# Performance work log

Measured on AMD Instinct MI355X. Metric: run time of the kernel, lower is better.

## Reference

```python
import jax, jax.numpy as jnp
import numpy as np

B, A, C_CLS = 64, 9, 20
H_FEAT, W_FEAT = 28, 28
IN_DIM, HID = 1280, 128
N_GT, M_POS = 40, 2048
AC5 = 5 * A + C_CLS


def setup_inputs() -> dict:
    key = jax.random.key(0)
    ks = jax.random.split(key, 10)
    features = jax.random.normal(ks[0], (B, IN_DIM, H_FEAT, W_FEAT), jnp.float32)
    # valid GT boxes in feature-map coordinates: (x1, y1, x2, y2, class)
    x1 = jax.random.uniform(ks[1], (B, N_GT), minval=0.0, maxval=W_FEAT - 6.0)
    y1 = jax.random.uniform(ks[2], (B, N_GT), minval=0.0, maxval=H_FEAT - 6.0)
    bw = jax.random.uniform(ks[3], (B, N_GT), minval=1.0, maxval=5.0)
    bh = jax.random.uniform(ks[4], (B, N_GT), minval=1.0, maxval=5.0)
    cls = jax.random.randint(ks[5], (B, N_GT), 0, C_CLS).astype(jnp.float32)
    bboxes = jnp.stack([x1, y1, x1 + bw, y1 + bh, cls], axis=-1)
    n_anchors_total = B * A * H_FEAT * W_FEAT
    pos_anchor_idx = jax.random.randint(ks[6], (M_POS,), 0, n_anchors_total, dtype=jnp.int32)
    neg_anchor_idx = jax.random.randint(ks[7], (M_POS,), 0, n_anchors_total, dtype=jnp.int32)
    W1 = jax.random.normal(ks[8], (HID, IN_DIM), jnp.float32) * 0.02
    b1 = jnp.zeros((HID,), jnp.float32)
    W2 = jax.random.normal(ks[9], (AC5, HID), jnp.float32) * 0.02
    b2 = jnp.zeros((AC5,), jnp.float32)
    anc = jnp.array([[1.0, 1], [2, 2], [3, 3], [4, 4], [5, 5], [2, 3], [3, 2], [3, 5], [5, 3]], jnp.float32)
    return dict(features=features, bboxes=bboxes, pos_anchor_idx=pos_anchor_idx,
                neg_anchor_idx=neg_anchor_idx, W1=W1, b1=b1, W2=W2, b2=b2, anc=anc)


def _detector_loss(features, bboxes, pos_idx, neg_idx, W1, b1, W2, b2, anc):
    Bx, _, Hf, Wf = features.shape
    N = bboxes.shape[1]
    Mp = pos_idx.shape[0]
    # ---- prediction network: two 1x1 convs (dropout skipped: eval mode) ----
    h = jnp.einsum('bchw,oc->bohw', features, W1) + b1[None, :, None, None]
    h = jax.nn.leaky_relu(h, 0.01)
    x = jnp.einsum('bchw,oc->bohw', h, W2) + b2[None, :, None, None]
    x_anchor = x[:, :5 * A].reshape(Bx, A, 5, Hf, Wf)  # (B,A,5,H,W)
    x_class = x[:, 5 * A:]                              # (B,C,H,W)
    # ---- GenerateGrid + GenerateAnchor ----
    xs = jnp.arange(Wf, dtype=jnp.float32) + 0.5
    ys = jnp.arange(Hf, dtype=jnp.float32) + 0.5
    gx, gy = jnp.meshgrid(xs, ys, indexing='xy')        # both (H,W)
    grid = jnp.stack([gx, gy], axis=-1)                 # (H,W,2)
    half = anc / 2.0                                    # (A,2)
    tl = grid[None] - half[:, None, None]               # (A,H,W,2)
    br = grid[None] + half[:, None, None]
    anchors = jnp.concatenate([tl, br], axis=-1)        # (A,H,W,4)
    p = jnp.broadcast_to(anchors[None], (Bx, A, Hf, Wf, 4)).reshape(Bx, -1, 4)  # (B,M,4)
    # ---- IoU matrix (B, M, N), exactly as source (signed w*h -> positive area) ----
    area_p = ((p[..., 0] - p[..., 2]) * (p[..., 1] - p[..., 3]))[:, :, None]
    area_b = ((bboxes[..., 2] - bboxes[..., 0]) * (bboxes[..., 3] - bboxes[..., 1]))[:, None, :]
    ix1 = jnp.maximum(p[:, :, None, 0], bboxes[:, None, :, 0])
    iy1 = jnp.maximum(p[:, :, None, 1], bboxes[:, None, :, 1])
    ix2 = jnp.minimum(p[:, :, None, 2], bboxes[:, None, :, 2])
    iy2 = jnp.minimum(p[:, :, None, 3], bboxes[:, None, :, 3])
    inter = jnp.clip(ix2 - ix1, 0.0) * jnp.clip(iy2 - iy1, 0.0)
    iou_mat = inter / (area_p + area_b - inter)          # (B,M,N)
    # ---- gather-based anchor/class extraction ----
    anc_data = jnp.transpose(x_anchor, (0, 1, 3, 4, 2)).reshape(-1, 5)  # (B*A*H*W, 5)
    pos_a = anc_data[pos_idx]
    neg_a = anc_data[neg_idx]
    conf_scores = jax.nn.sigmoid(jnp.concatenate([pos_a[:, 0], neg_a[:, 0]])[:, None])  # (2M,1)
    off = pos_a[:, 1:]
    offsets = jnp.concatenate([jax.nn.sigmoid(off[:, :2]) - 0.5, off[:, 2:]], axis=1)   # (M,4)
    cls_all = jnp.transpose(x_class, (0, 2, 3, 1))                       # (B,H,W,C)
    cls_all = jnp.broadcast_to(cls_all[:, None], (Bx, A, Hf, Wf, C_CLS)).reshape(-1, C_CLS)
    class_scores = cls_all[pos_idx]                                      # (M,C)
    # ---- match positives to GT via IoU argmax, build GT offsets/classes ----
    Mflat = A * Hf * Wf
    bpos = pos_idx // Mflat
    mpos = pos_idx % Mflat
    iou_pos = iou_mat[bpos, mpos]                 # (M,N)
    matched = jnp.argmax(iou_pos, axis=1)         # (M,)
    gt_box = bboxes[bpos, matched]                # (M,5)
    a_box = p[bpos, mpos]                         # (M,4)
    xa = 0.5 * (a_box[:, 0] + a_box[:, 2]); ya = 0.5 * (a_box[:, 1] + a_box[:, 3])
    wa = a_box[:, 2] - a_box[:, 0];          ha = a_box[:, 3] - a_box[:, 1]
    xb = 0.5 * (gt_box[:, 0] + gt_box[:, 2]); yb = 0.5 * (gt_box[:, 1] + gt_box[:, 3])
    wb = gt_box[:, 2] - gt_box[:, 0];          hb = gt_box[:, 3] - gt_box[:, 1]
    gt_offsets = jnp.stack([xb - xa, yb - ya, jnp.log(wb / wa), jnp.log(hb / ha)], axis=1)
    gt_offsets = jax.lax.stop_gradient(gt_offsets)
    gt_cls = gt_box[:, 4].astype(jnp.int32)
    # ---- losses (w_conf = w_reg = w_cls = 1) ----
    gt_conf = jnp.concatenate([jnp.ones((Mp, 1), jnp.float32), jnp.zeros((Mp, 1), jnp.float32)], axis=0)
    conf_loss = jnp.sum((conf_scores - gt_conf) ** 2) / (2.0 * Mp)
    reg_loss = jnp.sum((offsets - gt_offsets) ** 2) / Mp
    logp = jax.nn.log_softmax(class_scores, axis=-1)
    cls_loss = -jnp.mean(jnp.take_along_axis(logp, gt_cls[:, None], axis=1))
    return conf_loss + reg_loss + cls_loss


def reference(features, bboxes, pos_anchor_idx, neg_anchor_idx, W1, b1, W2, b2, anc):
    return _detector_loss(features, bboxes, pos_anchor_idx, neg_anchor_idx, W1, b1, W2, b2, anc)
```

## Files before the change

kernel.cpp:

```cpp
#include <hip/hip_runtime.h>
#include <math.h>

#define NPOS   2048
#define NANCH  4096
#define CIN    1280
#define HID    128
#define W_     28
#define HW_    784
#define AHW    7056
#define FB     (CIN*HW_)
#define SLAB   8
#define SLABF  (SLAB*HW_)

__device__ __forceinline__ float sigmoidf_(float x) {
    return 1.0f / (1.0f + __expf(-x));
}
__device__ __forceinline__ unsigned short f2bf(float x) {
    unsigned int u = __float_as_uint(x);
    return (unsigned short)((u + 0x7fffu + ((u >> 16) & 1u)) >> 16);
}
__device__ __forceinline__ float bf_lo(unsigned int w) { return __uint_as_float(w << 16); }
__device__ __forceinline__ float bf_hi(unsigned int w) { return __uint_as_float(w & 0xffff0000u); }

typedef __attribute__((address_space(3))) float lds_f;
typedef __attribute__((address_space(1))) const float glb_f;
__device__ __forceinline__ void gload16(const float* g, float* l) {
    __builtin_amdgcn_global_load_lds((glb_f*)g, (lds_f*)l, 16, 0, 0);
}

#define SCHED_FENCE() __builtin_amdgcn_sched_barrier(0)
#define WAIT_VM8()  asm volatile("s_waitcnt vmcnt(8)" ::: "memory")
#define WAIT_VM7()  asm volatile("s_waitcnt vmcnt(7)" ::: "memory")
#define WAIT_VM0()  asm volatile("s_waitcnt vmcnt(0)" ::: "memory")
#define WAIT_LGKM0() asm volatile("s_waitcnt lgkmcnt(0)" ::: "memory")

__global__ __launch_bounds__(256, 2) void k_fused(
    const float* __restrict__ F, const float* __restrict__ W1,
    const int* __restrict__ posi, const int* __restrict__ negi,
    unsigned short* __restrict__ Hp, int kchunk, int nslab)
{
    __shared__ float Pl[2][SLABF];
    __shared__ float Wl[2][1040];
    __shared__ float Gl[128][8];
    __shared__ int   pkl[128];
    __shared__ int   nbL;

    const int b    = blockIdx.x;
    const int ks   = blockIdx.y;
    const int t    = threadIdx.x;
    const int w    = t >> 6;
    const int lane = t & 63;

    if (t == 0) nbL = 0;
    if (t < 128) pkl[t] = 0;
    __syncthreads();
#pragma unroll
    for (int r = 0; r < 16; ++r) {
        const int g    = r * 256 + t;
        const int aidx = (g < NPOS) ? posi[g] : negi[g - NPOS];
        const int bb   = aidx / AHW;
        if (bb == b) {
            const int hw   = (aidx - bb * AHW) % HW_;
            const int slot = atomicAdd(&nbL, 1);
            if (slot < 128) pkl[slot] = (g << 10) | hw;
        }
    }
    __syncthreads();
    const int nb = nbL;

    const bool wact = (w * 32) < nb;
    const int  s_g  = w * 32 + (lane >> 1);
    const int  hh   = lane & 1;
    const int  a0   = w * 32 + (lane & 15) * 2;
    const int  og   = lane >> 4;

    float acc[2][32];
#pragma unroll
    for (int ai = 0; ai < 2; ++ai)
#pragma unroll
        for (int o = 0; o < 32; ++o) acc[ai][o] = 0.0f;

    const int kb0 = ks * kchunk;

    auto issue = [&](int sl2, int buf) {
        const int kb = kb0 + sl2 * SLAB;
        const float* srcP = F + (size_t)b * FB + (size_t)kb * HW_;
        float* dstP = &Pl[buf][0];
#pragma unroll
        for (int i = 0; i < 6; ++i) {
            const int c = w + 4 * i;
            gload16(srcP + c * 256 + lane * 4, dstP + c * 256);
        }
        if (w == 0 && lane < 32)
            gload16(srcP + 6144 + lane * 4, dstP + 6144);
        gload16(W1 + (size_t)(w * 32 + (lane >> 1)) * CIN + kb + 4 * (lane & 1),
                &Wl[buf][w * 260]);
    };

    issue(0, 0);
    issue(1, 1);
    SCHED_FENCE();
    if (w == 0) { WAIT_VM8(); } else { WAIT_VM7(); }
    SCHED_FENCE();
    __builtin_amdgcn_s_barrier();
    SCHED_FENCE();

    for (int sl = 0; sl < nslab; ++sl) {
        const int cur = sl & 1;
        if (wact) {
            const int  pk   = pkl[s_g];
            const int  hw   = pk & 1023;
            const bool real = (s_g < nb);
#pragma unroll
            for (int c = 0; c < 4; ++c) {
                const float v = Pl[cur][(4 * hh + c) * HW_ + hw];
                Gl[s_g][4 * hh + c] = real ? v : 0.0f;
            }
            const float4 gA0 = *(const float4*)&Gl[a0][0];
            const float4 gB0 = *(const float4*)&Gl[a0][4];
            const float4 gA1 = *(const float4*)&Gl[a0 + 1][0];
            const float4 gB1 = *(const float4*)&Gl[a0 + 1][4];
            const float* wbase = &Wl[cur][og * 260];
#pragma unroll
            for (int j = 0; j < 8; ++j) {
#pragma unroll
                for (int c = 0; c < 4; ++c) {
                    const int ol = 4 * j + c;
                    const float4 wA = *(const float4*)&wbase[ol * 8];
                    const float4 wB = *(const float4*)&wbase[ol * 8 + 4];
                    float v0 = acc[0][ol], v1 = acc[1][ol];
                    v0 = fmaf(gA0.x, wA.x, v0); v1 = fmaf(gA1.x, wA.x, v1);
                    v0 = fmaf(gA0.y, wA.y, v0); v1 = fmaf(gA1.y, wA.y, v1);
                    v0 = fmaf(gA0.z, wA.z, v0); v1 = fmaf(gA1.z, wA.z, v1);
                    v0 = fmaf(gA0.w, wA.w, v0); v1 = fmaf(gA1.w, wA.w, v1);
                    v0 = fmaf(gB0.x, wB.x, v0); v1 = fmaf(gB1.x, wB.x, v1);
                    v0 = fmaf(gB0.y, wB.y, v0); v1 = fmaf(gB1.y, wB.y, v1);
                    v0 = fmaf(gB0.z, wB.z, v0); v1 = fmaf(gB1.z, wB.z, v1);
                    v0 = fmaf(gB0.w, wB.w, v0); v1 = fmaf(gB1.w, wB.w, v1);
                    acc[0][ol] = v0; acc[1][ol] = v1;
                }
            }
        }
        if (sl + 1 < nslab) {
            WAIT_LGKM0();
            SCHED_FENCE();
            __builtin_amdgcn_s_barrier();
            SCHED_FENCE();
            if (sl + 2 < nslab) {
                issue(sl + 2, cur);
                SCHED_FENCE();
                if (w == 0) { WAIT_VM8(); } else { WAIT_VM7(); }
            } else {
                WAIT_VM0();
            }
            SCHED_FENCE();
            __builtin_amdgcn_s_barrier();
            SCHED_FENCE();
        }
    }

    if (wact) {
#pragma unroll
        for (int ai = 0; ai < 2; ++ai) {
            const int s = a0 + ai;
            if (s < nb) {
                const int g = pkl[s] >> 10;
                unsigned short* dst = Hp + ((size_t)ks * NANCH + g) * HID + og * 32;
                unsigned int u[16];
#pragma unroll
                for (int q = 0; q < 16; ++q)
                    u[q] = (unsigned)f2bf(acc[ai][2 * q]) |
                           ((unsigned)f2bf(acc[ai][2 * q + 1]) << 16);
#pragma unroll
                for (int q = 0; q < 4; ++q)
                    *(uint4*)(dst + 8 * q) =
                        make_uint4(u[4 * q], u[4 * q + 1], u[4 * q + 2], u[4 * q + 3]);
            }
        }
    }
}

__global__ __launch_bounds__(256) void k_loss(
    const unsigned short* __restrict__ Hp, const float* __restrict__ b1,
    int ksel, const float* __restrict__ W2, const float* __restrict__ b2,
    const int* __restrict__ posi, const int* __restrict__ negi,
    const float* __restrict__ bboxes, const float* __restrict__ anc,
    float* __restrict__ contrib)
{
    const int wid  = threadIdx.x >> 6;
    const int lane = threadIdx.x & 63;
    const int g    = blockIdx.x * 4 + wid;

    const int aidx = (g < NPOS) ? posi[g] : negi[g - NPOS];
    const int b   = aidx / AHW;
    const int rem = aidx - b * AHW;
    const int a   = rem / HW_;
    const int hw  = rem - a * HW_;
    const int hh  = hw / W_;
    const int ww  = hw - hh * W_;

    float hx = b1[2 * lane], hy = b1[2 * lane + 1];
    for (int ks = 0; ks < ksel; ++ks) {
        const unsigned raw =
            *(const unsigned*)&Hp[((size_t)ks * NANCH + g) * HID + 2 * lane];
        hx += bf_lo(raw);
        hy += bf_hi(raw);
    }
    hx = (hx > 0.0f) ? hx : 0.01f * hx;
    hy = (hy > 0.0f) ? hy : 0.01f * hy;

    if (g < NPOS) {
        float outv[25];
#pragma unroll
        for (int j = 0; j < 25; ++j) {
            const int row = (j < 5) ? (5 * a + j) : (40 + j);
            const float2 w = *(const float2*)&W2[(size_t)row * HID + 2 * lane];
            float v = fmaf(w.x, hx, w.y * hy);
#pragma unroll
            for (int off = 1; off < 64; off <<= 1) v += __shfl_xor(v, off, 64);
            outv[j] = v + b2[row];
        }

        const float wa = anc[2 * a], ha = anc[2 * a + 1];
        const float cx = ww + 0.5f, cy = hh + 0.5f;
        const float ax1 = cx - 0.5f * wa, ay1 = cy - 0.5f * ha;
        const float ax2 = cx + 0.5f * wa, ay2 = cy + 0.5f * ha;
        const float areap = wa * ha;

        float v; int vi = lane;
        if (lane < 40) {
            const float* bb = &bboxes[(size_t)(b * 40 + lane) * 5];
            const float bx1 = bb[0], by1 = bb[1], bx2 = bb[2], by2 = bb[3];
            const float areab = (bx2 - bx1) * (by2 - by1);
            const float ix1 = fmaxf(ax1, bx1), iy1 = fmaxf(ay1, by1);
            const float ix2 = fminf(ax2, bx2), iy2 = fminf(ay2, by2);
            const float inter = fmaxf(ix2 - ix1, 0.0f) * fmaxf(iy2 - iy1, 0.0f);
            v = inter / (areap + areab - inter);
        } else {
            v = -1.0f;
        }
#pragma unroll
        for (int off = 1; off < 64; off <<= 1) {
            const float ov = __shfl_xor(v, off, 64);
            const int   oi = __shfl_xor(vi, off, 64);
            if (ov > v || (ov == v && oi < vi)) { v = ov; vi = oi; }
        }
        const int m = vi;

        const float* gt = &bboxes[(size_t)(b * 40 + m) * 5];
        const float gx1 = gt[0], gy1 = gt[1], gx2 = gt[2], gy2 = gt[3];
        const int   gcls = (int)gt[4];
        const float xb = 0.5f * (gx1 + gx2), yb = 0.5f * (gy1 + gy2);
        const float wb = gx2 - gx1, hb = gy2 - gy1;
        const float go0 = xb - cx, go1 = yb - cy;
        const float go2 = __logf(wb / wa), go3 = __logf(hb / ha);

        const float o0 = sigmoidf_(outv[1]) - 0.5f;
        const float o1 = sigmoidf_(outv[2]) - 0.5f;
        const float o2 = outv[3], o3 = outv[4];
        const float reg = (o0 - go0) * (o0 - go0) + (o1 - go1) * (o1 - go1) +
                          (o2 - go2) * (o2 - go2) + (o3 - go3) * (o3 - go3);

        const float conf = sigmoidf_(outv[0]);
        const float conft = (conf - 1.0f) * (conf - 1.0f);

        float mx = outv[5];
#pragma unroll
        for (int c = 1; c < 20; ++c) mx = fmaxf(mx, outv[5 + c]);
        float se = 0.0f;
#pragma unroll
        for (int c = 0; c < 20; ++c) se += __expf(outv[5 + c] - mx);
        float lgt = 0.0f;
#pragma unroll
        for (int c = 0; c < 20; ++c) if (c == gcls) lgt = outv[5 + c];
        const float clst = -(lgt - mx - __logf(se));

        if (lane == 0)
            contrib[g] = conft * (1.0f / 4096.0f) + reg * (1.0f / 2048.0f) +
                         clst * (1.0f / 2048.0f);
    } else {
        const int row = 5 * a;
        const float2 w = *(const float2*)&W2[(size_t)row * HID + 2 * lane];
        float v = fmaf(w.x, hx, w.y * hy);
#pragma unroll
        for (int off = 1; off < 64; off <<= 1) v += __shfl_xor(v, off, 64);
        const float conf = sigmoidf_(v + b2[row]);
        if (lane == 0) contrib[g] = conf * conf * (1.0f / 4096.0f);
    }
}

__global__ __launch_bounds__(256) void k_final(const float* __restrict__ contrib,
                                               float* __restrict__ out)
{
    __shared__ float red[256];
    const int t = threadIdx.x;
    float s = 0.0f;
    for (int i = t; i < NANCH; i += 256) s += contrib[i];
    red[t] = s;
    __syncthreads();
    for (int st = 128; st > 0; st >>= 1) {
        if (t < st) red[t] += red[t + st];
        __syncthreads();
    }
    if (t == 0) out[0] = red[0];
}

extern "C" void kernel_launch(void* const* d_in, const int* in_sizes, int n_in,
                              void* d_out, int out_size, void* d_ws, size_t ws_size,
                              hipStream_t stream)
{
    const float* F      = (const float*)d_in[0];
    const float* bboxes = (const float*)d_in[1];
    const int*   posi   = (const int*)d_in[2];
    const int*   negi   = (const int*)d_in[3];
    const float* W1     = (const float*)d_in[4];
    const float* b1     = (const float*)d_in[5];
    const float* W2     = (const float*)d_in[6];
    const float* b2     = (const float*)d_in[7];
    const float* anc    = (const float*)d_in[8];
    float* out = (float*)d_out;

    char* ws = (char*)d_ws;
    int KSEL = 4;
    {
        const int opts[2] = {8, 4};
        for (int i = 0; i < 2; ++i) {
            size_t need = (size_t)opts[i] * NANCH * HID * 2 + (size_t)NANCH * 4 + 256;
            if (need <= ws_size) { KSEL = opts[i]; break; }
        }
    }
    unsigned short* Hp      = (unsigned short*)ws;
    float*          contrib = (float*)(ws + (size_t)KSEL * NANCH * HID * 2);

    const int kchunk = CIN / KSEL;
    const int nslab  = kchunk / SLAB;

    k_fused<<<dim3(64, KSEL), 256, 0, stream>>>(F, W1, posi, negi, Hp,
                                                kchunk, nslab);
    k_loss<<<NANCH / 4, 256, 0, stream>>>(Hp, b1, KSEL, W2, b2, posi, negi,
                                          bboxes, anc, contrib);
    k_final<<<1, 256, 0, stream>>>(contrib, out);
    (void)in_sizes; (void)n_in; (void)out_size;
}
```

Baseline: 85.96 us.

## Shrink slab, gather directly into registers, raise occupancy and split-K

The slab shrinks from 8 to 4 channels, and the Gl staging buffer is dropped so each thread gathers its four anchors' features straight from LDS into registers. The thread-to-output mapping moves to 4 anchors by 16 outputs with a rotated weight index, meant to avoid LDS bank conflicts. The first prefetches are now issued before the anchor-bucketing scan so the loads overlap it. Launch bounds rise to 4 blocks per CU, and split-K can go to 16 when workspace allows, which adds partial-sum traffic for k_loss.

Result: slower. 246.0 us (+186.2%).

```diff
diff --git a/kernel.cpp b/kernel.cpp
--- a/kernel.cpp
+++ b/kernel.cpp
@@ -9,7 +9,7 @@
 #define HW_    784
 #define AHW    7056
 #define FB     (CIN*HW_)
-#define SLAB   8
+#define SLAB   4
 #define SLABF  (SLAB*HW_)
 
 __device__ __forceinline__ float sigmoidf_(float x) {
@@ -29,19 +29,18 @@
 }
 
 #define SCHED_FENCE() __builtin_amdgcn_sched_barrier(0)
-#define WAIT_VM8()  asm volatile("s_waitcnt vmcnt(8)" ::: "memory")
-#define WAIT_VM7()  asm volatile("s_waitcnt vmcnt(7)" ::: "memory")
+#define WAIT_VM4()  asm volatile("s_waitcnt vmcnt(4)" ::: "memory")
+#define WAIT_VM3()  asm volatile("s_waitcnt vmcnt(3)" ::: "memory")
 #define WAIT_VM0()  asm volatile("s_waitcnt vmcnt(0)" ::: "memory")
 #define WAIT_LGKM0() asm volatile("s_waitcnt lgkmcnt(0)" ::: "memory")
 
-__global__ __launch_bounds__(256, 2) void k_fused(
+__global__ __launch_bounds__(256, 4) void k_fused(
     const float* __restrict__ F, const float* __restrict__ W1,
     const int* __restrict__ posi, const int* __restrict__ negi,
     unsigned short* __restrict__ Hp, int kchunk, int nslab)
 {
     __shared__ float Pl[2][SLABF];
-    __shared__ float Wl[2][1040];
-    __shared__ float Gl[128][8];
+    __shared__ float Wl[2][520];
     __shared__ int   pkl[128];
     __shared__ int   nbL;
 
@@ -54,6 +53,28 @@
     if (t == 0) nbL = 0;
     if (t < 128) pkl[t] = 0;
     __syncthreads();
+
+    const int kb0 = ks * kchunk;
+
+    auto issue = [&](int sl2, int buf) {
+        const int kb = kb0 + sl2 * SLAB;
+        const float* srcP = F + (size_t)b * FB + (size_t)kb * HW_;
+        float* dstP = &Pl[buf][0];
+#pragma unroll
+        for (int i = 0; i < 3; ++i) {
+            const int c = w + 4 * i;
+            gload16(srcP + c * 256 + lane * 4, dstP + c * 256);
+        }
+        if (w == 3) {
+            if (lane < 16) gload16(srcP + 3072 + lane * 4, dstP + 3072);
+        }
+        if (w == 1) gload16(W1 + (size_t)lane * CIN + kb, &Wl[buf][0]);
+        if (w == 2) gload16(W1 + (size_t)(64 + lane) * CIN + kb, &Wl[buf][260]);
+    };
+
+    issue(0, 0);
+    issue(1, 1);
+
 #pragma unroll
     for (int r = 0; r < 16; ++r) {
         const int g    = r * 256 + t;
@@ -65,79 +86,58 @@
             if (slot < 128) pkl[slot] = (g << 10) | hw;
         }
     }
-    __syncthreads();
-    const int nb = nbL;
-
-    const bool wact = (w * 32) < nb;
-    const int  s_g  = w * 32 + (lane >> 1);
-    const int  hh   = lane & 1;
-    const int  a0   = w * 32 + (lane & 15) * 2;
-    const int  og   = lane >> 4;
-
-    float acc[2][32];
-#pragma unroll
-    for (int ai = 0; ai < 2; ++ai)
-#pragma unroll
-        for (int o = 0; o < 32; ++o) acc[ai][o] = 0.0f;
-
-    const int kb0 = ks * kchunk;
-
-    auto issue = [&](int sl2, int buf) {
-        const int kb = kb0 + sl2 * SLAB;
-        const float* srcP = F + (size_t)b * FB + (size_t)kb * HW_;
-        float* dstP = &Pl[buf][0];
-#pragma unroll
-        for (int i = 0; i < 6; ++i) {
-            const int c = w + 4 * i;
-            gload16(srcP + c * 256 + lane * 4, dstP + c * 256);
-        }
-        if (w == 0 && lane < 32)
-            gload16(srcP + 6144 + lane * 4, dstP + 6144);
-        gload16(W1 + (size_t)(w * 32 + (lane >> 1)) * CIN + kb + 4 * (lane & 1),
-                &Wl[buf][w * 260]);
-    };
-
-    issue(0, 0);
-    issue(1, 1);
-    SCHED_FENCE();
-    if (w == 0) { WAIT_VM8(); } else { WAIT_VM7(); }
+    WAIT_LGKM0();
     SCHED_FENCE();
     __builtin_amdgcn_s_barrier();
     SCHED_FENCE();
 
+    const int  nb   = nbL;
+    const bool wact = (w * 32) < nb;
+    const int  og   = lane >> 3;
+    const int  al   = w * 32 + (lane & 7) * 4;
+    int hwr[4], gr[4];
+#pragma unroll
+    for (int ai = 0; ai < 4; ++ai) {
+        const int a  = al + ai;
+        const int pk = pkl[a];
+        hwr[ai] = pk & 1023;
+        gr[ai]  = (a < nb) ? (pk >> 10) : -1;
+    }
+    const int WB  = (og < 4) ? og * 64 : 260 + (og - 4) * 64;
+    const int rot = 2 * og;
+
+    float acc[4][16];
+#pragma unroll
+    for (int ai = 0; ai < 4; ++ai)
+#pragma unroll
+        for (int m = 0; m < 16; ++m) acc[ai][m] = 0.0f;
+
+    if (w == 0) { WAIT_VM3(); } else { WAIT_VM4(); }
+    SCHED_FENCE();
+    __builtin_amdgcn_s_barrier();
+    SCHED_FENCE();
+
     for (int sl = 0; sl < nslab; ++sl) {
         const int cur = sl & 1;
         if (wact) {
-            const int  pk   = pkl[s_g];
-            const int  hw   = pk & 1023;
-            const bool real = (s_g < nb);
-#pragma unroll
-            for (int c = 0; c < 4; ++c) {
-                const float v = Pl[cur][(4 * hh + c) * HW_ + hw];
-                Gl[s_g][4 * hh + c] = real ? v : 0.0f;
-            }
-            const float4 gA0 = *(const float4*)&Gl[a0][0];
-            const float4 gB0 = *(const float4*)&Gl[a0][4];
-            const float4 gA1 = *(const float4*)&Gl[a0 + 1][0];
-            const float4 gB1 = *(const float4*)&Gl[a0 + 1][4];
-            const float* wbase = &Wl[cur][og * 260];
-#pragma unroll
-            for (int j = 0; j < 8; ++j) {
-#pragma unroll
-                for (int c = 0; c < 4; ++c) {
-                    const int ol = 4 * j + c;
-                    const float4 wA = *(const float4*)&wbase[ol * 8];
-                    const float4 wB = *(const float4*)&wbase[ol * 8 + 4];
-                    float v0 = acc[0][ol], v1 = acc[1][ol];
-                    v0 = fmaf(gA0.x, wA.x, v0); v1 = fmaf(gA1.x, wA.x, v1);
-                    v0 = fmaf(gA0.y, wA.y, v0); v1 = fmaf(gA1.y, wA.y, v1);
-                    v0 = fmaf(gA0.z, wA.z, v0); v1 = fmaf(gA1.z, wA.z, v1);
-                    v0 = fmaf(gA0.w, wA.w, v0); v1 = fmaf(gA1.w, wA.w, v1);
-                    v0 = fmaf(gB0.x, wB.x, v0); v1 = fmaf(gB1.x, wB.x, v1);
-                    v0 = fmaf(gB0.y, wB.y, v0); v1 = fmaf(gB1.y, wB.y, v1);
-                    v0 = fmaf(gB0.z, wB.z, v0); v1 = fmaf(gB1.z, wB.z, v1);
-                    v0 = fmaf(gB0.w, wB.w, v0); v1 = fmaf(gB1.w, wB.w, v1);
-                    acc[0][ol] = v0; acc[1][ol] = v1;
+            float ga[4][4];
+#pragma unroll
+            for (int ai = 0; ai < 4; ++ai)
+#pragma unroll
+                for (int c = 0; c < 4; ++c)
+                    ga[ai][c] = Pl[cur][c * HW_ + hwr[ai]];
+#pragma unroll
+            for (int m = 0; m < 16; ++m) {
+                const float4 wv =
+                    *(const float4*)&Wl[cur][WB + 4 * ((m + rot) & 15)];
+#pragma unroll
+                for (int ai = 0; ai < 4; ++ai) {
+                    float v = acc[ai][m];
+                    v = fmaf(ga[ai][0], wv.x, v);
+                    v = fmaf(ga[ai][1], wv.y, v);
+                    v = fmaf(ga[ai][2], wv.z, v);
+                    v = fmaf(ga[ai][3], wv.w, v);
+                    acc[ai][m] = v;
                 }
             }
         }
@@ -149,7 +149,7 @@
             if (sl + 2 < nslab) {
                 issue(sl + 2, cur);
                 SCHED_FENCE();
-                if (w == 0) { WAIT_VM8(); } else { WAIT_VM7(); }
+                if (w == 0) { WAIT_VM3(); } else { WAIT_VM4(); }
             } else {
                 WAIT_VM0();
             }
@@ -161,20 +161,20 @@
 
     if (wact) {
 #pragma unroll
-        for (int ai = 0; ai < 2; ++ai) {
-            const int s = a0 + ai;
-            if (s < nb) {
-                const int g = pkl[s] >> 10;
-                unsigned short* dst = Hp + ((size_t)ks * NANCH + g) * HID + og * 32;
-                unsigned int u[16];
-#pragma unroll
-                for (int q = 0; q < 16; ++q)
-                    u[q] = (unsigned)f2bf(acc[ai][2 * q]) |
-                           ((unsigned)f2bf(acc[ai][2 * q + 1]) << 16);
-#pragma unroll
-                for (int q = 0; q < 4; ++q)
-                    *(uint4*)(dst + 8 * q) =
-                        make_uint4(u[4 * q], u[4 * q + 1], u[4 * q + 2], u[4 * q + 3]);
+        for (int ai = 0; ai < 4; ++ai) {
+            const int g = gr[ai];
+            if (g >= 0) {
+                unsigned short* dst =
+                    Hp + ((size_t)ks * NANCH + g) * HID + og * 16;
+                unsigned u[8];
+#pragma unroll
+                for (int q = 0; q < 8; ++q) {
+                    const int m0 = (2 * q - rot) & 15;
+                    u[q] = (unsigned)f2bf(acc[ai][m0]) |
+                           ((unsigned)f2bf(acc[ai][m0 + 1]) << 16);
+                }
+                *(uint4*)(dst)     = make_uint4(u[0], u[1], u[2], u[3]);
+                *(uint4*)(dst + 8) = make_uint4(u[4], u[5], u[6], u[7]);
             }
         }
     }
@@ -323,8 +323,8 @@
     char* ws = (char*)d_ws;
     int KSEL = 4;
     {
-        const int opts[2] = {8, 4};
-        for (int i = 0; i < 2; ++i) {
+        const int opts[3] = {16, 8, 4};
+        for (int i = 0; i < 3; ++i) {
             size_t need = (size_t)opts[i] * NANCH * HID * 2 + (size_t)NANCH * 4 + 256;
             if (need <= ws_size) { KSEL = opts[i]; break; }
         }
```
